# Optimization experiments

Measured on AMD Instinct MI355X. Metric: run time of the kernel, lower is better.

## Reference

```python
import jax, jax.numpy as jnp
import numpy as np

B = 262144   # number of (group, item) prediction pairs
M = 16       # max members per group (ragged -> padded)
NU = 100000  # num_users
NI = 50000   # num_items
D = 32       # embedding_dim (hardcoded via torch.zeros([32]))


def setup_inputs() -> dict:
    key = jax.random.key(0)
    ks = jax.random.split(key, 9)
    item_inputs = jax.random.randint(ks[0], (B,), 0, NI)
    member_ids = jax.random.randint(ks[1], (B, M), 0, NU)
    lengths = jax.random.randint(ks[2], (B, 1), 1, M + 1)
    member_mask = jnp.arange(M)[None, :] < lengths  # [B, M] bool, variable group sizes
    user_table = jax.random.normal(ks[3], (NU, D), jnp.float32) * 0.1  # xavier-ish
    item_table = jax.random.normal(ks[4], (NI, D), jnp.float32) * 0.1
    W_bil = jax.random.normal(ks[5], (D, D), jnp.float32)  # nn.Bilinear(D, D, 1) weight[0]
    b_bil = jax.random.normal(ks[6], (1,), jnp.float32) * 0.05
    W1 = jax.random.normal(ks[7], (8, 3 * D), jnp.float32) * 0.05  # Linear(96, 8)
    b1 = jnp.zeros((8,), jnp.float32)
    W2 = jax.random.normal(ks[8], (1, 8), jnp.float32) * 0.05  # Linear(8, 1)
    b2 = jnp.zeros((1,), jnp.float32)
    return {
        "item_inputs": item_inputs, "member_ids": member_ids, "member_mask": member_mask,
        "user_table": user_table, "item_table": item_table,
        "W_bil": W_bil, "b_bil": b_bil, "W1": W1, "b1": b1, "W2": W2, "b2": b2,
    }


def reference(item_inputs, member_ids, member_mask, user_table, item_table,
              W_bil, b_bil, W1, b1, W2, b2):
    item_e = item_table[item_inputs]          # [B, D] gather
    mem_e = user_table[member_ids]            # [B, M, D] gather
    # bilinear attention score per member: m^T W i + b (softmax in original is computed then discarded)
    scores = jnp.einsum('bmd,de,be->bm', mem_e, W_bil, item_e) + b_bil[0]
    w = scores * member_mask.astype(scores.dtype)  # zero out padded members (ragged groups)
    final_user = jnp.einsum('bm,bmd->bd', w, mem_e)  # unnormalized weighted sum of members
    new_embeds = jnp.concatenate([final_user * item_e, final_user, item_e], axis=-1)  # [B, 3D]
    h = jax.nn.relu(new_embeds @ W1.T + b1)
    y = jax.nn.sigmoid(h @ W2.T + b2)          # [B, 1]
    return y
```

## Files before the change

### kernel.cpp

```cpp
#include <hip/hip_runtime.h>
#include <math.h>

#define DD 32
#define MM 16
#define TROW 40

__device__ __forceinline__ void load8f4(const float* __restrict__ p, float* r) {
    const float4* q = (const float4*)p;
#pragma unroll
    for (int i = 0; i < 8; ++i) {
        float4 v = q[i];
        r[4*i+0] = v.x; r[4*i+1] = v.y; r[4*i+2] = v.z; r[4*i+3] = v.w;
    }
}

__global__ void precompute_item(const float* __restrict__ item_table,
                                const float* __restrict__ W_bil,
                                const float* __restrict__ W1,
                                float* __restrict__ tbl, int NI) {
    int i = blockIdx.x * blockDim.x + threadIdx.x;
    if (i >= NI) return;
    float it[DD];
    load8f4(item_table + (size_t)i * DD, it);
    float* o = tbl + (size_t)i * TROW;
#pragma unroll 4
    for (int d = 0; d < DD; ++d) {
        float s = 0.f;
#pragma unroll
        for (int e = 0; e < DD; ++e) s = fmaf(W_bil[d * DD + e], it[e], s);
        o[d] = s;
    }
#pragma unroll
    for (int j = 0; j < 8; ++j) {
        float s = 0.f;
#pragma unroll
        for (int d = 0; d < DD; ++d) s = fmaf(W1[j * 96 + 64 + d], it[d], s);
        o[32 + j] = s;
    }
}

template <bool USE_TBL>
__global__ __launch_bounds__(256)
void bilinear_main(const int* __restrict__ item_inputs,
                   const int* __restrict__ member_ids,
                   const unsigned char* __restrict__ member_mask,
                   const float* __restrict__ user_table,
                   const float* __restrict__ item_table,
                   const float* __restrict__ tbl,
                   const float* __restrict__ W_bil,
                   const float* __restrict__ b_bil,
                   const float* __restrict__ W1,
                   const float* __restrict__ b1v,
                   const float* __restrict__ W2,
                   const float* __restrict__ b2v,
                   float* __restrict__ out, int Btot) {
    int tid = blockIdx.x * blockDim.x + threadIdx.x;
    int b = tid >> 2;
    if (b >= Btot) return;
    int q  = tid & 3;
    int ko = q * 8;

    int item = item_inputs[b];

    const uint4 mv = *(const uint4*)(member_mask + (size_t)b * MM);
    int len = __popc(mv.x & 0x01010101u) + __popc(mv.y & 0x01010101u) +
              __popc(mv.z & 0x01010101u) + __popc(mv.w & 0x01010101u);

    float t[8];
    if (USE_TBL) {
        const float4* tp = (const float4*)(tbl + (size_t)item * TROW + ko);
        float4 a = tp[0], c = tp[1];
        t[0]=a.x; t[1]=a.y; t[2]=a.z; t[3]=a.w; t[4]=c.x; t[5]=c.y; t[6]=c.z; t[7]=c.w;
    } else {
        float itf[DD];
        load8f4(item_table + (size_t)item * DD, itf);
#pragma unroll
        for (int k = 0; k < 8; ++k) {
            const float* w = W_bil + (ko + k) * DD;
            float s0 = 0.f, s1 = 0.f, s2 = 0.f, s3 = 0.f;
#pragma unroll
            for (int e = 0; e < DD; e += 4) {
                s0 = fmaf(w[e+0], itf[e+0], s0);
                s1 = fmaf(w[e+1], itf[e+1], s1);
                s2 = fmaf(w[e+2], itf[e+2], s2);
                s3 = fmaf(w[e+3], itf[e+3], s3);
            }
            t[k] = (s0 + s1) + (s2 + s3);
        }
    }

    float bb = b_bil[0];
    float fin[8];
#pragma unroll
    for (int k = 0; k < 8; ++k) fin[k] = 0.f;

    const int* idp = member_ids + (size_t)b * MM;
    int id = idp[0];
    for (int m = 0; m < len; ++m) {
        int idn = idp[(m + 1) & (MM - 1)];
        const float4* up = (const float4*)(user_table + (size_t)id * DD + ko);
        float4 a = up[0], c = up[1];
        float me0 = a.x, me1 = a.y, me2 = a.z, me3 = a.w;
        float me4 = c.x, me5 = c.y, me6 = c.z, me7 = c.w;
        float s0 = fmaf(me0, t[0], fmaf(me1, t[1], 0.f));
        float s1 = fmaf(me2, t[2], fmaf(me3, t[3], 0.f));
        float s2 = fmaf(me4, t[4], fmaf(me5, t[5], 0.f));
        float s3 = fmaf(me6, t[6], fmaf(me7, t[7], 0.f));
        float s = (s0 + s1) + (s2 + s3);
        s += __shfl_xor(s, 1);
        s += __shfl_xor(s, 2);
        s += bb;
        fin[0] = fmaf(s, me0, fin[0]); fin[1] = fmaf(s, me1, fin[1]);
        fin[2] = fmaf(s, me2, fin[2]); fin[3] = fmaf(s, me3, fin[3]);
        fin[4] = fmaf(s, me4, fin[4]); fin[5] = fmaf(s, me5, fin[5]);
        fin[6] = fmaf(s, me6, fin[6]); fin[7] = fmaf(s, me7, fin[7]);
        id = idn;
    }

    const float4* ip = (const float4*)(item_table + (size_t)item * DD + ko);
    float4 ia = ip[0], ic = ip[1];
    float it8[8] = {ia.x, ia.y, ia.z, ia.w, ic.x, ic.y, ic.z, ic.w};

    float p8[8];
#pragma unroll
    for (int k = 0; k < 8; ++k) p8[k] = fin[k] * it8[k];

    float u[8];
#pragma unroll
    for (int j = 0; j < 8; ++j) {
        const float* wr = W1 + j * 96 + ko;
        float4 wa0 = *(const float4*)(wr);
        float4 wa1 = *(const float4*)(wr + 4);
        float4 wb0 = *(const float4*)(wr + 32);
        float4 wb1 = *(const float4*)(wr + 36);
        float x = 0.f, y = 0.f;
        x = fmaf(wa0.x, p8[0], x); y = fmaf(wb0.x, fin[0], y);
        x = fmaf(wa0.y, p8[1], x); y = fmaf(wb0.y, fin[1], y);
        x = fmaf(wa0.z, p8[2], x); y = fmaf(wb0.z, fin[2], y);
        x = fmaf(wa0.w, p8[3], x); y = fmaf(wb0.w, fin[3], y);
        x = fmaf(wa1.x, p8[4], x); y = fmaf(wb1.x, fin[4], y);
        x = fmaf(wa1.y, p8[5], x); y = fmaf(wb1.y, fin[5], y);
        x = fmaf(wa1.z, p8[6], x); y = fmaf(wb1.z, fin[6], y);
        x = fmaf(wa1.w, p8[7], x); y = fmaf(wb1.w, fin[7], y);
        u[j] = x + y;
    }
#pragma unroll
    for (int j = 0; j < 8; ++j) {
        u[j] += __shfl_xor(u[j], 1);
        u[j] += __shfl_xor(u[j], 2);
    }

    if (q == 0) {
        float cj[8];
        if (USE_TBL) {
            const float4* cp = (const float4*)(tbl + (size_t)item * TROW + 32);
            float4 ca = cp[0], cb = cp[1];
            cj[0]=ca.x; cj[1]=ca.y; cj[2]=ca.z; cj[3]=ca.w;
            cj[4]=cb.x; cj[5]=cb.y; cj[6]=cb.z; cj[7]=cb.w;
        } else {
            float itf[DD];
            load8f4(item_table + (size_t)item * DD, itf);
#pragma unroll
            for (int j = 0; j < 8; ++j) {
                float s = 0.f;
#pragma unroll
                for (int d = 0; d < DD; ++d) s = fmaf(W1[j * 96 + 64 + d], itf[d], s);
                cj[j] = s;
            }
        }
        float z = b2v[0];
#pragma unroll
        for (int j = 0; j < 8; ++j) {
            float hv = u[j] + cj[j] + b1v[j];
            hv = hv > 0.f ? hv : 0.f;
            z = fmaf(W2[j], hv, z);
        }
        __builtin_nontemporal_store(1.f / (1.f + __expf(-z)), out + b);
    }
}

extern "C" void kernel_launch(void* const* d_in, const int* in_sizes, int n_in,
                              void* d_out, int out_size, void* d_ws, size_t ws_size,
                              hipStream_t stream) {
    const int*           item_inputs = (const int*)d_in[0];
    const int*           member_ids  = (const int*)d_in[1];
    const unsigned char* member_mask = (const unsigned char*)d_in[2];
    const float*         user_table  = (const float*)d_in[3];
    const float*         item_table  = (const float*)d_in[4];
    const float*         W_bil       = (const float*)d_in[5];
    const float*         b_bil       = (const float*)d_in[6];
    const float*         W1          = (const float*)d_in[7];
    const float*         b1          = (const float*)d_in[8];
    const float*         W2          = (const float*)d_in[9];
    const float*         b2          = (const float*)d_in[10];
    float* out = (float*)d_out;

    int Btot = in_sizes[0];
    int NI   = in_sizes[4] / DD;

    bool use_tbl = ws_size >= (size_t)NI * TROW * sizeof(float);
    int blk = 256;
    long long nthreads = (long long)Btot * 4;
    if (use_tbl) {
        float* tbl = (float*)d_ws;
        precompute_item<<<(NI + blk - 1) / blk, blk, 0, stream>>>(item_table, W_bil, W1, tbl, NI);
        bilinear_main<true><<<(int)((nthreads + blk - 1) / blk), blk, 0, stream>>>(
            item_inputs, member_ids, member_mask, user_table, item_table, tbl,
            W_bil, b_bil, W1, b1, W2, b2, out, Btot);
    } else {
        bilinear_main<false><<<(int)((nthreads + blk - 1) / blk), blk, 0, stream>>>(
            item_inputs, member_ids, member_mask, user_table, item_table, nullptr,
            W_bil, b_bil, W1, b1, W2, b2, out, Btot);
    }
}
```

Before: 154.6 us.

## Store user table and item precompute table in fp16 to halve gather bytes

Adds a per-call pass that converts the user embedding table to fp16, and changes the item precompute table to fp16 so it also holds the item embedding row. The main kernel then gathers half-width rows, with the member loop unrolled by two so more loads are in flight. This targets the memory traffic of the random gathers. In exchange it adds a full user-table conversion pass on every call and introduces fp16 rounding into embeddings and intermediate products.

```diff
diff --git a/kernel.cpp b/kernel.cpp
--- a/kernel.cpp
+++ b/kernel.cpp
@@ -3,7 +3,10 @@
 
 #define DD 32
 #define MM 16
-#define TROW 40
+#define TROWH 80
+
+typedef _Float16 half8 __attribute__((ext_vector_type(8)));
+typedef _Float16 half2t __attribute__((ext_vector_type(2)));
 
 __device__ __forceinline__ void load8f4(const float* __restrict__ p, float* r) {
     const float4* q = (const float4*)p;
@@ -14,80 +17,102 @@
     }
 }
 
+__device__ __forceinline__ float dot8(const float* a, const float* b) {
+    float s0 = fmaf(a[0], b[0], fmaf(a[1], b[1], 0.f));
+    float s1 = fmaf(a[2], b[2], fmaf(a[3], b[3], 0.f));
+    float s2 = fmaf(a[4], b[4], fmaf(a[5], b[5], 0.f));
+    float s3 = fmaf(a[6], b[6], fmaf(a[7], b[7], 0.f));
+    return (s0 + s1) + (s2 + s3);
+}
+
+__global__ void convert_user(const float* __restrict__ ut, _Float16* __restrict__ o, int n8) {
+    int g = blockIdx.x * blockDim.x + threadIdx.x;
+    if (g >= n8) return;
+    const float4* p = (const float4*)ut + 2 * (size_t)g;
+    float4 a = p[0], b = p[1];
+    half8 h;
+    h[0] = (_Float16)a.x; h[1] = (_Float16)a.y; h[2] = (_Float16)a.z; h[3] = (_Float16)a.w;
+    h[4] = (_Float16)b.x; h[5] = (_Float16)b.y; h[6] = (_Float16)b.z; h[7] = (_Float16)b.w;
+    *((half8*)o + g) = h;
+}
+
 __global__ void precompute_item(const float* __restrict__ item_table,
                                 const float* __restrict__ W_bil,
                                 const float* __restrict__ W1,
-                                float* __restrict__ tbl, int NI) {
-    int i = blockIdx.x * blockDim.x + threadIdx.x;
+                                _Float16* __restrict__ tbl, int NI) {
+    int g = blockIdx.x * blockDim.x + threadIdx.x;
+    int i = g >> 2, q = g & 3;
     if (i >= NI) return;
+    int ko = q * 8;
+    const float* row = item_table + (size_t)i * DD;
     float it[DD];
-    load8f4(item_table + (size_t)i * DD, it);
-    float* o = tbl + (size_t)i * TROW;
-#pragma unroll 4
-    for (int d = 0; d < DD; ++d) {
-        float s = 0.f;
-#pragma unroll
-        for (int e = 0; e < DD; ++e) s = fmaf(W_bil[d * DD + e], it[e], s);
-        o[d] = s;
-    }
-#pragma unroll
-    for (int j = 0; j < 8; ++j) {
-        float s = 0.f;
-#pragma unroll
-        for (int d = 0; d < DD; ++d) s = fmaf(W1[j * 96 + 64 + d], it[d], s);
-        o[32 + j] = s;
-    }
-}
-
-template <bool USE_TBL>
+    load8f4(row, it);
+    _Float16* o = tbl + (size_t)i * TROWH;
+
+    half8 th;
+#pragma unroll
+    for (int k = 0; k < 8; ++k) {
+        const float* w = W_bil + (ko + k) * DD;
+        float s0 = 0.f, s1 = 0.f, s2 = 0.f, s3 = 0.f;
+#pragma unroll
+        for (int e = 0; e < DD; e += 4) {
+            s0 = fmaf(w[e+0], it[e+0], s0);
+            s1 = fmaf(w[e+1], it[e+1], s1);
+            s2 = fmaf(w[e+2], it[e+2], s2);
+            s3 = fmaf(w[e+3], it[e+3], s3);
+        }
+        th[k] = (_Float16)((s0 + s1) + (s2 + s3));
+    }
+    *(half8*)(o + ko) = th;
+
+    {
+        const float4* ip = (const float4*)(row + ko);
+        float4 a = ip[0], c = ip[1];
+        half8 ih;
+        ih[0] = (_Float16)a.x; ih[1] = (_Float16)a.y; ih[2] = (_Float16)a.z; ih[3] = (_Float16)a.w;
+        ih[4] = (_Float16)c.x; ih[5] = (_Float16)c.y; ih[6] = (_Float16)c.z; ih[7] = (_Float16)c.w;
+        *(half8*)(o + DD + ko) = ih;
+    }
+
+    int j0 = 2 * q;
+    float c0 = 0.f, c1 = 0.f;
+#pragma unroll
+    for (int e = 0; e < DD; ++e) {
+        c0 = fmaf(W1[j0 * 96 + 64 + e], it[e], c0);
+        c1 = fmaf(W1[(j0 + 1) * 96 + 64 + e], it[e], c1);
+    }
+    half2t ch; ch[0] = (_Float16)c0; ch[1] = (_Float16)c1;
+    *(half2t*)(o + 64 + 2 * q) = ch;
+}
+
 __global__ __launch_bounds__(256)
-void bilinear_main(const int* __restrict__ item_inputs,
-                   const int* __restrict__ member_ids,
-                   const unsigned char* __restrict__ member_mask,
-                   const float* __restrict__ user_table,
-                   const float* __restrict__ item_table,
-                   const float* __restrict__ tbl,
-                   const float* __restrict__ W_bil,
-                   const float* __restrict__ b_bil,
-                   const float* __restrict__ W1,
-                   const float* __restrict__ b1v,
-                   const float* __restrict__ W2,
-                   const float* __restrict__ b2v,
-                   float* __restrict__ out, int Btot) {
+void bilinear_main_h(const int* __restrict__ item_inputs,
+                     const int* __restrict__ member_ids,
+                     const unsigned char* __restrict__ member_mask,
+                     const _Float16* __restrict__ ut_h,
+                     const _Float16* __restrict__ tbl,
+                     const float* __restrict__ b_bil,
+                     const float* __restrict__ W1,
+                     const float* __restrict__ b1v,
+                     const float* __restrict__ W2,
+                     const float* __restrict__ b2v,
+                     float* __restrict__ out, int Btot) {
     int tid = blockIdx.x * blockDim.x + threadIdx.x;
     int b = tid >> 2;
     if (b >= Btot) return;
-    int q  = tid & 3;
+    int q = tid & 3;
     int ko = q * 8;
 
     int item = item_inputs[b];
-
     const uint4 mv = *(const uint4*)(member_mask + (size_t)b * MM);
     int len = __popc(mv.x & 0x01010101u) + __popc(mv.y & 0x01010101u) +
               __popc(mv.z & 0x01010101u) + __popc(mv.w & 0x01010101u);
 
+    const _Float16* tb = tbl + (size_t)item * TROWH;
+    half8 th = *(const half8*)(tb + ko);
     float t[8];
-    if (USE_TBL) {
-        const float4* tp = (const float4*)(tbl + (size_t)item * TROW + ko);
-        float4 a = tp[0], c = tp[1];
-        t[0]=a.x; t[1]=a.y; t[2]=a.z; t[3]=a.w; t[4]=c.x; t[5]=c.y; t[6]=c.z; t[7]=c.w;
-    } else {
-        float itf[DD];
-        load8f4(item_table + (size_t)item * DD, itf);
-#pragma unroll
-        for (int k = 0; k < 8; ++k) {
-            const float* w = W_bil + (ko + k) * DD;
-            float s0 = 0.f, s1 = 0.f, s2 = 0.f, s3 = 0.f;
-#pragma unroll
-            for (int e = 0; e < DD; e += 4) {
-                s0 = fmaf(w[e+0], itf[e+0], s0);
-                s1 = fmaf(w[e+1], itf[e+1], s1);
-                s2 = fmaf(w[e+2], itf[e+2], s2);
-                s3 = fmaf(w[e+3], itf[e+3], s3);
-            }
-            t[k] = (s0 + s1) + (s2 + s3);
-        }
-    }
+#pragma unroll
+    for (int k = 0; k < 8; ++k) t[k] = (float)th[k];
 
     float bb = b_bil[0];
     float fin[8];
@@ -95,31 +120,39 @@
     for (int k = 0; k < 8; ++k) fin[k] = 0.f;
 
     const int* idp = member_ids + (size_t)b * MM;
-    int id = idp[0];
-    for (int m = 0; m < len; ++m) {
-        int idn = idp[(m + 1) & (MM - 1)];
-        const float4* up = (const float4*)(user_table + (size_t)id * DD + ko);
-        float4 a = up[0], c = up[1];
-        float me0 = a.x, me1 = a.y, me2 = a.z, me3 = a.w;
-        float me4 = c.x, me5 = c.y, me6 = c.z, me7 = c.w;
-        float s0 = fmaf(me0, t[0], fmaf(me1, t[1], 0.f));
-        float s1 = fmaf(me2, t[2], fmaf(me3, t[3], 0.f));
-        float s2 = fmaf(me4, t[4], fmaf(me5, t[5], 0.f));
-        float s3 = fmaf(me6, t[6], fmaf(me7, t[7], 0.f));
-        float s = (s0 + s1) + (s2 + s3);
-        s += __shfl_xor(s, 1);
-        s += __shfl_xor(s, 2);
-        s += bb;
-        fin[0] = fmaf(s, me0, fin[0]); fin[1] = fmaf(s, me1, fin[1]);
-        fin[2] = fmaf(s, me2, fin[2]); fin[3] = fmaf(s, me3, fin[3]);
-        fin[4] = fmaf(s, me4, fin[4]); fin[5] = fmaf(s, me5, fin[5]);
-        fin[6] = fmaf(s, me6, fin[6]); fin[7] = fmaf(s, me7, fin[7]);
-        id = idn;
-    }
-
-    const float4* ip = (const float4*)(item_table + (size_t)item * DD + ko);
-    float4 ia = ip[0], ic = ip[1];
-    float it8[8] = {ia.x, ia.y, ia.z, ia.w, ic.x, ic.y, ic.z, ic.w};
+    int m = 0;
+    for (; m + 2 <= len; m += 2) {
+        int ida = idp[m], idb = idp[m + 1];
+        half8 ha = *(const half8*)(ut_h + (size_t)ida * DD + ko);
+        half8 hb = *(const half8*)(ut_h + (size_t)idb * DD + ko);
+        float ma[8], mc[8];
+#pragma unroll
+        for (int k = 0; k < 8; ++k) { ma[k] = (float)ha[k]; mc[k] = (float)hb[k]; }
+        float sa = dot8(ma, t);
+        float sb = dot8(mc, t);
+        sa += __shfl_xor(sa, 1); sa += __shfl_xor(sa, 2);
+        sb += __shfl_xor(sb, 1); sb += __shfl_xor(sb, 2);
+        sa += bb; sb += bb;
+#pragma unroll
+        for (int k = 0; k < 8; ++k) fin[k] = fmaf(sb, mc[k], fmaf(sa, ma[k], fin[k]));
+    }
+    if (m < len) {
+        int ida = idp[m];
+        half8 ha = *(const half8*)(ut_h + (size_t)ida * DD + ko);
+        float ma[8];
+#pragma unroll
+        for (int k = 0; k < 8; ++k) ma[k] = (float)ha[k];
+        float sa = dot8(ma, t);
+        sa += __shfl_xor(sa, 1); sa += __shfl_xor(sa, 2);
+        sa += bb;
+#pragma unroll
+        for (int k = 0; k < 8; ++k) fin[k] = fmaf(sa, ma[k], fin[k]);
+    }
+
+    half8 ih = *(const half8*)(tb + DD + ko);
+    float it8[8];
+#pragma unroll
+    for (int k = 0; k < 8; ++k) it8[k] = (float)ih[k];
 
     float p8[8];
 #pragma unroll
@@ -151,27 +184,117 @@
     }
 
     if (q == 0) {
-        float cj[8];
-        if (USE_TBL) {
-            const float4* cp = (const float4*)(tbl + (size_t)item * TROW + 32);
-            float4 ca = cp[0], cb = cp[1];
-            cj[0]=ca.x; cj[1]=ca.y; cj[2]=ca.z; cj[3]=ca.w;
-            cj[4]=cb.x; cj[5]=cb.y; cj[6]=cb.z; cj[7]=cb.w;
-        } else {
-            float itf[DD];
-            load8f4(item_table + (size_t)item * DD, itf);
-#pragma unroll
-            for (int j = 0; j < 8; ++j) {
-                float s = 0.f;
-#pragma unroll
-                for (int d = 0; d < DD; ++d) s = fmaf(W1[j * 96 + 64 + d], itf[d], s);
-                cj[j] = s;
-            }
+        half8 ch = *(const half8*)(tb + 64);
+        float z = b2v[0];
+#pragma unroll
+        for (int j = 0; j < 8; ++j) {
+            float hv = u[j] + (float)ch[j] + b1v[j];
+            hv = hv > 0.f ? hv : 0.f;
+            z = fmaf(W2[j], hv, z);
         }
+        __builtin_nontemporal_store(1.f / (1.f + __expf(-z)), out + b);
+    }
+}
+
+__global__ __launch_bounds__(256)
+void bilinear_main_f(const int* __restrict__ item_inputs,
+                     const int* __restrict__ member_ids,
+                     const unsigned char* __restrict__ member_mask,
+                     const float* __restrict__ user_table,
+                     const float* __restrict__ item_table,
+                     const float* __restrict__ W_bil,
+                     const float* __restrict__ b_bil,
+                     const float* __restrict__ W1,
+                     const float* __restrict__ b1v,
+                     const float* __restrict__ W2,
+                     const float* __restrict__ b2v,
+                     float* __restrict__ out, int Btot) {
+    int tid = blockIdx.x * blockDim.x + threadIdx.x;
+    int b = tid >> 2;
+    if (b >= Btot) return;
+    int q = tid & 3;
+    int ko = q * 8;
+
+    int item = item_inputs[b];
+    const uint4 mv = *(const uint4*)(member_mask + (size_t)b * MM);
+    int len = __popc(mv.x & 0x01010101u) + __popc(mv.y & 0x01010101u) +
+              __popc(mv.z & 0x01010101u) + __popc(mv.w & 0x01010101u);
+
+    float itf[DD];
+    load8f4(item_table + (size_t)item * DD, itf);
+    float t[8];
+#pragma unroll
+    for (int k = 0; k < 8; ++k) {
+        const float* w = W_bil + (ko + k) * DD;
+        float s0 = 0.f, s1 = 0.f, s2 = 0.f, s3 = 0.f;
+#pragma unroll
+        for (int e = 0; e < DD; e += 4) {
+            s0 = fmaf(w[e+0], itf[e+0], s0);
+            s1 = fmaf(w[e+1], itf[e+1], s1);
+            s2 = fmaf(w[e+2], itf[e+2], s2);
+            s3 = fmaf(w[e+3], itf[e+3], s3);
+        }
+        t[k] = (s0 + s1) + (s2 + s3);
+    }
+
+    float bb = b_bil[0];
+    float fin[8];
+#pragma unroll
+    for (int k = 0; k < 8; ++k) fin[k] = 0.f;
+
+    const int* idp = member_ids + (size_t)b * MM;
+    for (int m = 0; m < len; ++m) {
+        int id = idp[m];
+        const float4* up = (const float4*)(user_table + (size_t)id * DD + ko);
+        float4 a = up[0], c = up[1];
+        float me[8] = {a.x, a.y, a.z, a.w, c.x, c.y, c.z, c.w};
+        float s = dot8(me, t);
+        s += __shfl_xor(s, 1); s += __shfl_xor(s, 2);
+        s += bb;
+#pragma unroll
+        for (int k = 0; k < 8; ++k) fin[k] = fmaf(s, me[k], fin[k]);
+    }
+
+    const float4* ip = (const float4*)(item_table + (size_t)item * DD + ko);
+    float4 ia = ip[0], ic = ip[1];
+    float it8[8] = {ia.x, ia.y, ia.z, ia.w, ic.x, ic.y, ic.z, ic.w};
+    float p8[8];
+#pragma unroll
+    for (int k = 0; k < 8; ++k) p8[k] = fin[k] * it8[k];
+
+    float u[8];
+#pragma unroll
+    for (int j = 0; j < 8; ++j) {
+        const float* wr = W1 + j * 96 + ko;
+        float4 wa0 = *(const float4*)(wr);
+        float4 wa1 = *(const float4*)(wr + 4);
+        float4 wb0 = *(const float4*)(wr + 32);
+        float4 wb1 = *(const float4*)(wr + 36);
+        float x = 0.f, y = 0.f;
+        x = fmaf(wa0.x, p8[0], x); y = fmaf(wb0.x, fin[0], y);
+        x = fmaf(wa0.y, p8[1], x); y = fmaf(wb0.y, fin[1], y);
+        x = fmaf(wa0.z, p8[2], x); y = fmaf(wb0.z, fin[2], y);
+        x = fmaf(wa0.w, p8[3], x); y = fmaf(wb0.w, fin[3], y);
+        x = fmaf(wa1.x, p8[4], x); y = fmaf(wb1.x, fin[4], y);
+        x = fmaf(wa1.y, p8[5], x); y = fmaf(wb1.y, fin[5], y);
+        x = fmaf(wa1.z, p8[6], x); y = fmaf(wb1.z, fin[6], y);
+        x = fmaf(wa1.w, p8[7], x); y = fmaf(wb1.w, fin[7], y);
+        u[j] = x + y;
+    }
+#pragma unroll
+    for (int j = 0; j < 8; ++j) {
+        u[j] += __shfl_xor(u[j], 1);
+        u[j] += __shfl_xor(u[j], 2);
+    }
+
+    if (q == 0) {
         float z = b2v[0];
 #pragma unroll
         for (int j = 0; j < 8; ++j) {
-            float hv = u[j] + cj[j] + b1v[j];
+            float cj = 0.f;
+#pragma unroll
+            for (int d = 0; d < DD; ++d) cj = fmaf(W1[j * 96 + 64 + d], itf[d], cj);
+            float hv = u[j] + cj + b1v[j];
             hv = hv > 0.f ? hv : 0.f;
             z = fmaf(W2[j], hv, z);
         }
@@ -196,20 +319,27 @@
     float* out = (float*)d_out;
 
     int Btot = in_sizes[0];
+    int NU   = in_sizes[3] / DD;
     int NI   = in_sizes[4] / DD;
 
-    bool use_tbl = ws_size >= (size_t)NI * TROW * sizeof(float);
+    size_t tbl_bytes = (size_t)NI * TROWH * sizeof(_Float16);
+    size_t ut_off    = (tbl_bytes + 255) & ~(size_t)255;
+    size_t need      = ut_off + (size_t)NU * DD * sizeof(_Float16);
+
     int blk = 256;
     long long nthreads = (long long)Btot * 4;
-    if (use_tbl) {
-        float* tbl = (float*)d_ws;
-        precompute_item<<<(NI + blk - 1) / blk, blk, 0, stream>>>(item_table, W_bil, W1, tbl, NI);
-        bilinear_main<true><<<(int)((nthreads + blk - 1) / blk), blk, 0, stream>>>(
-            item_inputs, member_ids, member_mask, user_table, item_table, tbl,
+    if (ws_size >= need) {
+        _Float16* tbl  = (_Float16*)d_ws;
+        _Float16* ut_h = (_Float16*)((char*)d_ws + ut_off);
+        int n8 = NU * DD / 8;
+        convert_user<<<(n8 + blk - 1) / blk, blk, 0, stream>>>(user_table, ut_h, n8);
+        precompute_item<<<(NI * 4 + blk - 1) / blk, blk, 0, stream>>>(item_table, W_bil, W1, tbl, NI);
+        bilinear_main_h<<<(int)((nthreads + blk - 1) / blk), blk, 0, stream>>>(
+            item_inputs, member_ids, member_mask, ut_h, tbl,
+            b_bil, W1, b1, W2, b2, out, Btot);
+    } else {
+        bilinear_main_f<<<(int)((nthreads + blk - 1) / blk), blk, 0, stream>>>(
+            item_inputs, member_ids, member_mask, user_table, item_table,
             W_bil, b_bil, W1, b1, W2, b2, out, Btot);
-    } else {
-        bilinear_main<false><<<(int)((nthreads + blk - 1) / blk), blk, 0, stream>>>(
-            item_inputs, member_ids, member_mask, user_table, item_table, nullptr,
-            W_bil, b_bil, W1, b1, W2, b2, out, Btot);
-    }
-}
+    }
+}
```

Result: slower. 173.4 us (+12.1%).

## Gather user embeddings from fp16 copy and drop item precompute table

Applied to the files above, without the earlier changes.

Replaces the per-item precompute table with a pre-pass that converts the user table to fp16 in workspace, so member gathers read half the bytes. The bilinear item projection W_bil·item is now recomputed per thread from the item row. The W1 item term is folded into the distributed per-lane dot product instead of being computed serially by lane 0. The member loop is unrolled by two to overlap gathers, and the item index is loaded nontemporally. This trades fp16 rounding of user embeddings and extra per-row compute for less gather traffic, and the conversion pass reads the whole user table on every call.

```diff
diff --git a/kernel.cpp b/kernel.cpp
--- a/kernel.cpp
+++ b/kernel.cpp
@@ -3,7 +3,8 @@
 
 #define DD 32
 #define MM 16
-#define TROW 40
+
+typedef _Float16 half8 __attribute__((ext_vector_type(8)));
 
 __device__ __forceinline__ void load8f4(const float* __restrict__ p, float* r) {
     const float4* q = (const float4*)p;
@@ -14,39 +15,36 @@
     }
 }
 
-__global__ void precompute_item(const float* __restrict__ item_table,
-                                const float* __restrict__ W_bil,
-                                const float* __restrict__ W1,
-                                float* __restrict__ tbl, int NI) {
-    int i = blockIdx.x * blockDim.x + threadIdx.x;
-    if (i >= NI) return;
-    float it[DD];
-    load8f4(item_table + (size_t)i * DD, it);
-    float* o = tbl + (size_t)i * TROW;
-#pragma unroll 4
-    for (int d = 0; d < DD; ++d) {
-        float s = 0.f;
-#pragma unroll
-        for (int e = 0; e < DD; ++e) s = fmaf(W_bil[d * DD + e], it[e], s);
-        o[d] = s;
-    }
-#pragma unroll
-    for (int j = 0; j < 8; ++j) {
-        float s = 0.f;
-#pragma unroll
-        for (int d = 0; d < DD; ++d) s = fmaf(W1[j * 96 + 64 + d], it[d], s);
-        o[32 + j] = s;
-    }
-}
-
-template <bool USE_TBL>
+__device__ __forceinline__ float dot8f(const float* a, const float* b) {
+    float s0 = fmaf(a[0], b[0], fmaf(a[1], b[1], 0.f));
+    float s1 = fmaf(a[2], b[2], fmaf(a[3], b[3], 0.f));
+    float s2 = fmaf(a[4], b[4], fmaf(a[5], b[5], 0.f));
+    float s3 = fmaf(a[6], b[6], fmaf(a[7], b[7], 0.f));
+    return (s0 + s1) + (s2 + s3);
+}
+
+__global__ void convert_user(const float* __restrict__ ut, _Float16* __restrict__ o, int n16) {
+    int g = blockIdx.x * blockDim.x + threadIdx.x;
+    if (g >= n16) return;
+    const float4* p = (const float4*)ut + 4 * (size_t)g;
+    float4 a = p[0], b = p[1], c = p[2], d = p[3];
+    half8 h0, h1;
+    h0[0] = (_Float16)a.x; h0[1] = (_Float16)a.y; h0[2] = (_Float16)a.z; h0[3] = (_Float16)a.w;
+    h0[4] = (_Float16)b.x; h0[5] = (_Float16)b.y; h0[6] = (_Float16)b.z; h0[7] = (_Float16)b.w;
+    h1[0] = (_Float16)c.x; h1[1] = (_Float16)c.y; h1[2] = (_Float16)c.z; h1[3] = (_Float16)c.w;
+    h1[4] = (_Float16)d.x; h1[5] = (_Float16)d.y; h1[6] = (_Float16)d.z; h1[7] = (_Float16)d.w;
+    half8* q = (half8*)o + 2 * (size_t)g;
+    q[0] = h0; q[1] = h1;
+}
+
+template <bool H>
 __global__ __launch_bounds__(256)
 void bilinear_main(const int* __restrict__ item_inputs,
                    const int* __restrict__ member_ids,
                    const unsigned char* __restrict__ member_mask,
                    const float* __restrict__ user_table,
+                   const _Float16* __restrict__ ut_h,
                    const float* __restrict__ item_table,
-                   const float* __restrict__ tbl,
                    const float* __restrict__ W_bil,
                    const float* __restrict__ b_bil,
                    const float* __restrict__ W1,
@@ -57,36 +55,30 @@
     int tid = blockIdx.x * blockDim.x + threadIdx.x;
     int b = tid >> 2;
     if (b >= Btot) return;
-    int q  = tid & 3;
+    int q = tid & 3;
     int ko = q * 8;
 
-    int item = item_inputs[b];
-
+    int item = __builtin_nontemporal_load(item_inputs + b);
     const uint4 mv = *(const uint4*)(member_mask + (size_t)b * MM);
     int len = __popc(mv.x & 0x01010101u) + __popc(mv.y & 0x01010101u) +
               __popc(mv.z & 0x01010101u) + __popc(mv.w & 0x01010101u);
 
+    float itf[DD];
+    load8f4(item_table + (size_t)item * DD, itf);
+
     float t[8];
-    if (USE_TBL) {
-        const float4* tp = (const float4*)(tbl + (size_t)item * TROW + ko);
-        float4 a = tp[0], c = tp[1];
-        t[0]=a.x; t[1]=a.y; t[2]=a.z; t[3]=a.w; t[4]=c.x; t[5]=c.y; t[6]=c.z; t[7]=c.w;
-    } else {
-        float itf[DD];
-        load8f4(item_table + (size_t)item * DD, itf);
-#pragma unroll
-        for (int k = 0; k < 8; ++k) {
-            const float* w = W_bil + (ko + k) * DD;
-            float s0 = 0.f, s1 = 0.f, s2 = 0.f, s3 = 0.f;
-#pragma unroll
-            for (int e = 0; e < DD; e += 4) {
-                s0 = fmaf(w[e+0], itf[e+0], s0);
-                s1 = fmaf(w[e+1], itf[e+1], s1);
-                s2 = fmaf(w[e+2], itf[e+2], s2);
-                s3 = fmaf(w[e+3], itf[e+3], s3);
-            }
-            t[k] = (s0 + s1) + (s2 + s3);
-        }
+#pragma unroll
+    for (int k = 0; k < 8; ++k) {
+        const float* w = W_bil + (ko + k) * DD;
+        float s0 = 0.f, s1 = 0.f, s2 = 0.f, s3 = 0.f;
+#pragma unroll
+        for (int e = 0; e < DD; e += 4) {
+            s0 = fmaf(w[e+0], itf[e+0], s0);
+            s1 = fmaf(w[e+1], itf[e+1], s1);
+            s2 = fmaf(w[e+2], itf[e+2], s2);
+            s3 = fmaf(w[e+3], itf[e+3], s3);
+        }
+        t[k] = (s0 + s1) + (s2 + s3);
     }
 
     float bb = b_bil[0];
@@ -95,32 +87,57 @@
     for (int k = 0; k < 8; ++k) fin[k] = 0.f;
 
     const int* idp = member_ids + (size_t)b * MM;
-    int id = idp[0];
-    for (int m = 0; m < len; ++m) {
-        int idn = idp[(m + 1) & (MM - 1)];
-        const float4* up = (const float4*)(user_table + (size_t)id * DD + ko);
-        float4 a = up[0], c = up[1];
-        float me0 = a.x, me1 = a.y, me2 = a.z, me3 = a.w;
-        float me4 = c.x, me5 = c.y, me6 = c.z, me7 = c.w;
-        float s0 = fmaf(me0, t[0], fmaf(me1, t[1], 0.f));
-        float s1 = fmaf(me2, t[2], fmaf(me3, t[3], 0.f));
-        float s2 = fmaf(me4, t[4], fmaf(me5, t[5], 0.f));
-        float s3 = fmaf(me6, t[6], fmaf(me7, t[7], 0.f));
-        float s = (s0 + s1) + (s2 + s3);
-        s += __shfl_xor(s, 1);
-        s += __shfl_xor(s, 2);
-        s += bb;
-        fin[0] = fmaf(s, me0, fin[0]); fin[1] = fmaf(s, me1, fin[1]);
-        fin[2] = fmaf(s, me2, fin[2]); fin[3] = fmaf(s, me3, fin[3]);
-        fin[4] = fmaf(s, me4, fin[4]); fin[5] = fmaf(s, me5, fin[5]);
-        fin[6] = fmaf(s, me6, fin[6]); fin[7] = fmaf(s, me7, fin[7]);
-        id = idn;
+    int m = 0;
+    for (; m + 2 <= len; m += 2) {
+        int ida = idp[m], idb = idp[m + 1];
+        float ma[8], mc[8];
+        if (H) {
+            half8 ha = *(const half8*)(ut_h + (size_t)ida * DD + ko);
+            half8 hb = *(const half8*)(ut_h + (size_t)idb * DD + ko);
+#pragma unroll
+            for (int k = 0; k < 8; ++k) { ma[k] = (float)ha[k]; mc[k] = (float)hb[k]; }
+        } else {
+            const float4* ua = (const float4*)(user_table + (size_t)ida * DD + ko);
+            const float4* ub = (const float4*)(user_table + (size_t)idb * DD + ko);
+            float4 a0 = ua[0], a1 = ua[1], b0 = ub[0], b1 = ub[1];
+            ma[0]=a0.x; ma[1]=a0.y; ma[2]=a0.z; ma[3]=a0.w;
+            ma[4]=a1.x; ma[5]=a1.y; ma[6]=a1.z; ma[7]=a1.w;
+            mc[0]=b0.x; mc[1]=b0.y; mc[2]=b0.z; mc[3]=b0.w;
+            mc[4]=b1.x; mc[5]=b1.y; mc[6]=b1.z; mc[7]=b1.w;
+        }
+        float sa = dot8f(ma, t);
+        float sb = dot8f(mc, t);
+        sa += __shfl_xor(sa, 1); sb += __shfl_xor(sb, 1);
+        sa += __shfl_xor(sa, 2); sb += __shfl_xor(sb, 2);
+        sa += bb; sb += bb;
+#pragma unroll
+        for (int k = 0; k < 8; ++k)
+            fin[k] = fmaf(sb, mc[k], fmaf(sa, ma[k], fin[k]));
+    }
+    if (m < len) {
+        int ida = idp[m];
+        float ma[8];
+        if (H) {
+            half8 ha = *(const half8*)(ut_h + (size_t)ida * DD + ko);
+#pragma unroll
+            for (int k = 0; k < 8; ++k) ma[k] = (float)ha[k];
+        } else {
+            const float4* ua = (const float4*)(user_table + (size_t)ida * DD + ko);
+            float4 a0 = ua[0], a1 = ua[1];
+            ma[0]=a0.x; ma[1]=a0.y; ma[2]=a0.z; ma[3]=a0.w;
+            ma[4]=a1.x; ma[5]=a1.y; ma[6]=a1.z; ma[7]=a1.w;
+        }
+        float sa = dot8f(ma, t);
+        sa += __shfl_xor(sa, 1);
+        sa += __shfl_xor(sa, 2);
+        sa += bb;
+#pragma unroll
+        for (int k = 0; k < 8; ++k) fin[k] = fmaf(sa, ma[k], fin[k]);
     }
 
     const float4* ip = (const float4*)(item_table + (size_t)item * DD + ko);
     float4 ia = ip[0], ic = ip[1];
     float it8[8] = {ia.x, ia.y, ia.z, ia.w, ic.x, ic.y, ic.z, ic.w};
-
     float p8[8];
 #pragma unroll
     for (int k = 0; k < 8; ++k) p8[k] = fin[k] * it8[k];
@@ -133,16 +150,18 @@
         float4 wa1 = *(const float4*)(wr + 4);
         float4 wb0 = *(const float4*)(wr + 32);
         float4 wb1 = *(const float4*)(wr + 36);
-        float x = 0.f, y = 0.f;
-        x = fmaf(wa0.x, p8[0], x); y = fmaf(wb0.x, fin[0], y);
-        x = fmaf(wa0.y, p8[1], x); y = fmaf(wb0.y, fin[1], y);
-        x = fmaf(wa0.z, p8[2], x); y = fmaf(wb0.z, fin[2], y);
-        x = fmaf(wa0.w, p8[3], x); y = fmaf(wb0.w, fin[3], y);
-        x = fmaf(wa1.x, p8[4], x); y = fmaf(wb1.x, fin[4], y);
-        x = fmaf(wa1.y, p8[5], x); y = fmaf(wb1.y, fin[5], y);
-        x = fmaf(wa1.z, p8[6], x); y = fmaf(wb1.z, fin[6], y);
-        x = fmaf(wa1.w, p8[7], x); y = fmaf(wb1.w, fin[7], y);
-        u[j] = x + y;
+        float4 wc0 = *(const float4*)(wr + 64);
+        float4 wc1 = *(const float4*)(wr + 68);
+        float x = 0.f, y = 0.f, v = 0.f;
+        x = fmaf(wa0.x, p8[0], x); y = fmaf(wb0.x, fin[0], y); v = fmaf(wc0.x, it8[0], v);
+        x = fmaf(wa0.y, p8[1], x); y = fmaf(wb0.y, fin[1], y); v = fmaf(wc0.y, it8[1], v);
+        x = fmaf(wa0.z, p8[2], x); y = fmaf(wb0.z, fin[2], y); v = fmaf(wc0.z, it8[2], v);
+        x = fmaf(wa0.w, p8[3], x); y = fmaf(wb0.w, fin[3], y); v = fmaf(wc0.w, it8[3], v);
+        x = fmaf(wa1.x, p8[4], x); y = fmaf(wb1.x, fin[4], y); v = fmaf(wc1.x, it8[4], v);
+        x = fmaf(wa1.y, p8[5], x); y = fmaf(wb1.y, fin[5], y); v = fmaf(wc1.y, it8[5], v);
+        x = fmaf(wa1.z, p8[6], x); y = fmaf(wb1.z, fin[6], y); v = fmaf(wc1.z, it8[6], v);
+        x = fmaf(wa1.w, p8[7], x); y = fmaf(wb1.w, fin[7], y); v = fmaf(wc1.w, it8[7], v);
+        u[j] = (x + y) + v;
     }
 #pragma unroll
     for (int j = 0; j < 8; ++j) {
@@ -151,27 +170,10 @@
     }
 
     if (q == 0) {
-        float cj[8];
-        if (USE_TBL) {
-            const float4* cp = (const float4*)(tbl + (size_t)item * TROW + 32);
-            float4 ca = cp[0], cb = cp[1];
-            cj[0]=ca.x; cj[1]=ca.y; cj[2]=ca.z; cj[3]=ca.w;
-            cj[4]=cb.x; cj[5]=cb.y; cj[6]=cb.z; cj[7]=cb.w;
-        } else {
-            float itf[DD];
-            load8f4(item_table + (size_t)item * DD, itf);
-#pragma unroll
-            for (int j = 0; j < 8; ++j) {
-                float s = 0.f;
-#pragma unroll
-                for (int d = 0; d < DD; ++d) s = fmaf(W1[j * 96 + 64 + d], itf[d], s);
-                cj[j] = s;
-            }
-        }
         float z = b2v[0];
 #pragma unroll
         for (int j = 0; j < 8; ++j) {
-            float hv = u[j] + cj[j] + b1v[j];
+            float hv = u[j] + b1v[j];
             hv = hv > 0.f ? hv : 0.f;
             z = fmaf(W2[j], hv, z);
         }
@@ -196,20 +198,22 @@
     float* out = (float*)d_out;
 
     int Btot = in_sizes[0];
-    int NI   = in_sizes[4] / DD;
-
-    bool use_tbl = ws_size >= (size_t)NI * TROW * sizeof(float);
+    int NU   = in_sizes[3] / DD;
+
+    size_t need = (size_t)NU * DD * sizeof(_Float16);
+
     int blk = 256;
     long long nthreads = (long long)Btot * 4;
-    if (use_tbl) {
-        float* tbl = (float*)d_ws;
-        precompute_item<<<(NI + blk - 1) / blk, blk, 0, stream>>>(item_table, W_bil, W1, tbl, NI);
+    if (ws_size >= need) {
+        _Float16* ut_h = (_Float16*)d_ws;
+        int n16 = NU * DD / 16;
+        convert_user<<<(n16 + blk - 1) / blk, blk, 0, stream>>>(user_table, ut_h, n16);
         bilinear_main<true><<<(int)((nthreads + blk - 1) / blk), blk, 0, stream>>>(
-            item_inputs, member_ids, member_mask, user_table, item_table, tbl,
+            item_inputs, member_ids, member_mask, user_table, ut_h, item_table,
             W_bil, b_bil, W1, b1, W2, b2, out, Btot);
     } else {
         bilinear_main<false><<<(int)((nthreads + blk - 1) / blk), blk, 0, stream>>>(
-            item_inputs, member_ids, member_mask, user_table, item_table, nullptr,
+            item_inputs, member_ids, member_mask, user_table, nullptr, item_table,
             W_bil, b_bil, W1, b1, W2, b2, out, Btot);
     }
 }
```

New measurement: 252.5 us. 1.63x slower.
